# Optimization experiments

Measured on AMD Instinct MI355X. Metric: run time of the kernel, lower is better.

Reference implementation:

```python
import jax, jax.numpy as jnp
import numpy as np

BN_EPS = 1e-5
N_OUT, D_OUT = 64, 128


def setup_inputs() -> dict:
    key = jax.random.key(0)
    k1, k2, k3, k4 = jax.random.split(key, 4)
    B, N_in, D_in, K = 512, 64, 128, 4
    x = jax.random.normal(k1, (B, N_in, D_in), dtype=jnp.float32)
    # block-sparse weights: one (D_in x D_out) block per (output-row, active-input-row) pair
    W = jax.random.normal(k2, (N_OUT, K, D_in, D_OUT), dtype=jnp.float32) * (1.0 / np.sqrt(K * D_in))
    bias = jax.random.normal(k3, (N_OUT, D_OUT), dtype=jnp.float32) * 0.02
    gamma = jnp.ones((N_OUT * D_OUT,), dtype=jnp.float32)
    beta = jnp.zeros((N_OUT * D_OUT,), dtype=jnp.float32)
    idx = jax.random.randint(k4, (N_OUT, K), 0, N_in, dtype=jnp.int32)
    return {"x": x, "W": W, "bias": bias, "gamma": gamma, "beta": beta, "idx": idx}


def reference(x, W, bias, gamma, beta, idx):
    B = x.shape[0]
    # structured-sparse linear: gather active input rows, per-block matmul
    xg = x[:, idx, :]                                   # [B, N_out, K, D_in]
    y = jnp.einsum('bokd,okde->boe', xg, W) + bias      # [B, N_out, D_out]
    # BatchNorm1d (training-mode batch statistics) on flattened features
    yf = y.reshape(B, -1)                               # [B, N_out*D_out]
    mean = jnp.mean(yf, axis=0)
    var = jnp.mean(jnp.square(yf - mean), axis=0)       # biased variance, as in torch BN
    yn = (yf - mean) * jax.lax.rsqrt(var + BN_EPS) * gamma + beta
    # Swish: z * sigmoid(z)
    out = yn * jax.nn.sigmoid(yn)
    return out.reshape(B, N_OUT, D_OUT)
```

## Files before the change

kernel.cpp:

```cpp
#include <hip/hip_runtime.h>


typedef __attribute__((ext_vector_type(8))) __bf16 bf16x8;
typedef __attribute__((ext_vector_type(4))) __bf16 bf16x4;
typedef __attribute__((ext_vector_type(4))) float  f32x4;

#define B_SZ   512
#define N_IN   64
#define D_IN   128
#define N_O    64
#define D_O    128
#define FEAT   (N_O * D_O)
#define LDA    40

__global__ __launch_bounds__(1024, 4)
void fused_encoder_kernel(const float* __restrict__ x, const float* __restrict__ W,
                          const float* __restrict__ bias, const float* __restrict__ gamma,
                          const float* __restrict__ beta, const int* __restrict__ idxp,
                          float* __restrict__ out)
{
    __shared__ __bf16 Alds[512 * LDA];
    __shared__ __bf16 Blds[128 * LDA];
    __shared__ float  Sred[8 * 128];
    __shared__ float  Qred[8 * 128];
    __shared__ float  sscale[128];
    __shared__ float  sshift[128];

    const int o    = blockIdx.x;
    const int tid  = threadIdx.x;
    const int wave = tid >> 6;
    const int lane = tid & 63;
    const int wr   = wave >> 1;
    const int wc   = wave & 1;
    const int lam  = lane & 15;
    const int quad = lane >> 4;

    int rsel[4];
#pragma unroll
    for (int k = 0; k < 4; ++k) rsel[k] = idxp[o * 4 + k];

    const f32x4 zero4 = {0.f, 0.f, 0.f, 0.f};
    f32x4 acc[4][4];
#pragma unroll
    for (int mi = 0; mi < 4; ++mi)
#pragma unroll
        for (int ni = 0; ni < 4; ++ni) acc[mi][ni] = zero4;

    const int m_a = tid >> 1;
    const int ca  = (tid & 1) * 16;
    const int e_b = tid & 127;
    const int dgb = tid >> 7;

    for (int kk = 0; kk < 16; ++kk) {
        const int kidx = kk >> 2;
        const int d0   = (kk & 3) * 32;
        const int r    = rsel[kidx];

        const float* xa = x + ((m_a * N_IN + r) * D_IN + d0 + ca);
        f32x4 xv0 = *(const f32x4*)(xa + 0);
        f32x4 xv1 = *(const f32x4*)(xa + 4);
        f32x4 xv2 = *(const f32x4*)(xa + 8);
        f32x4 xv3 = *(const f32x4*)(xa + 12);
        bf16x8 p0, p1;
        p0[0] = (__bf16)xv0[0]; p0[1] = (__bf16)xv0[1];
        p0[2] = (__bf16)xv0[2]; p0[3] = (__bf16)xv0[3];
        p0[4] = (__bf16)xv1[0]; p0[5] = (__bf16)xv1[1];
        p0[6] = (__bf16)xv1[2]; p0[7] = (__bf16)xv1[3];
        p1[0] = (__bf16)xv2[0]; p1[1] = (__bf16)xv2[1];
        p1[2] = (__bf16)xv2[2]; p1[3] = (__bf16)xv2[3];
        p1[4] = (__bf16)xv3[0]; p1[5] = (__bf16)xv3[1];
        p1[6] = (__bf16)xv3[2]; p1[7] = (__bf16)xv3[3];

        const float* wp = W + (((o * 4 + kidx) * 128 + (d0 + dgb * 4)) * 128 + e_b);
        bf16x4 wb;
        wb[0] = (__bf16)wp[0];
        wb[1] = (__bf16)wp[128];
        wb[2] = (__bf16)wp[256];
        wb[3] = (__bf16)wp[384];

        __syncthreads();
        *(bf16x8*)&Alds[m_a * LDA + ca]     = p0;
        *(bf16x8*)&Alds[m_a * LDA + ca + 8] = p1;
        *(bf16x4*)&Blds[e_b * LDA + dgb * 4] = wb;
        __syncthreads();

        bf16x8 af[4], bfv[4];
#pragma unroll
        for (int mi = 0; mi < 4; ++mi)
            af[mi] = *(const bf16x8*)&Alds[(wr * 64 + mi * 16 + lam) * LDA + quad * 8];
#pragma unroll
        for (int ni = 0; ni < 4; ++ni)
            bfv[ni] = *(const bf16x8*)&Blds[(wc * 64 + ni * 16 + lam) * LDA + quad * 8];
#pragma unroll
        for (int mi = 0; mi < 4; ++mi)
#pragma unroll
            for (int ni = 0; ni < 4; ++ni)
                acc[mi][ni] = __builtin_amdgcn_mfma_f32_16x16x32_bf16(
                    af[mi], bfv[ni], acc[mi][ni], 0, 0, 0);
    }

    const int nbase = wc * 64;
    float bvals[4];
#pragma unroll
    for (int ni = 0; ni < 4; ++ni)
        bvals[ni] = bias[o * 128 + nbase + ni * 16 + lam];
#pragma unroll
    for (int mi = 0; mi < 4; ++mi)
#pragma unroll
        for (int ni = 0; ni < 4; ++ni)
#pragma unroll
            for (int rr = 0; rr < 4; ++rr) acc[mi][ni][rr] += bvals[ni];

#pragma unroll
    for (int ni = 0; ni < 4; ++ni) {
        float s = 0.f, q = 0.f;
#pragma unroll
        for (int mi = 0; mi < 4; ++mi)
#pragma unroll
            for (int rr = 0; rr < 4; ++rr) {
                const float v = acc[mi][ni][rr];
                s += v; q += v * v;
            }
        s += __shfl_xor(s, 16); s += __shfl_xor(s, 32);
        q += __shfl_xor(q, 16); q += __shfl_xor(q, 32);
        if (quad == 0) {
            const int e = nbase + ni * 16 + lam;
            Sred[wr * 128 + e] = s;
            Qred[wr * 128 + e] = q;
        }
    }
    __syncthreads();

    if (tid < 128) {
        float s = 0.f, q = 0.f;
#pragma unroll
        for (int sl = 0; sl < 8; ++sl) {
            s += Sred[sl * 128 + tid];
            q += Qred[sl * 128 + tid];
        }
        const float mean = s * (1.0f / 512.0f);
        const float var  = q * (1.0f / 512.0f) - mean * mean;
        const float rstd = rsqrtf(var + 1e-5f);
        const float sc   = rstd * gamma[o * 128 + tid];
        sscale[tid] = sc;
        sshift[tid] = beta[o * 128 + tid] - mean * sc;
    }
    __syncthreads();

#pragma unroll
    for (int mi = 0; mi < 4; ++mi) {
        const int rowb = wr * 64 + mi * 16 + quad * 4;
#pragma unroll
        for (int ni = 0; ni < 4; ++ni) {
            const int col = nbase + ni * 16 + lam;
            const float sc = sscale[col];
            const float sh = sshift[col];
#pragma unroll
            for (int rr = 0; rr < 4; ++rr) {
                const float xn = acc[mi][ni][rr] * sc + sh;
                const float sg = 1.0f / (1.0f + __expf(-xn));
                out[(rowb + rr) * FEAT + o * 128 + col] = xn * sg;
            }
        }
    }
}

extern "C" void kernel_launch(void* const* d_in, const int* in_sizes, int n_in,
                              void* d_out, int out_size, void* d_ws, size_t ws_size,
                              hipStream_t stream)
{
    const float* x     = (const float*)d_in[0];
    const float* W     = (const float*)d_in[1];
    const float* bias  = (const float*)d_in[2];
    const float* gamma = (const float*)d_in[3];
    const float* beta  = (const float*)d_in[4];
    const int*   idx   = (const int*)d_in[5];
    float* out = (float*)d_out;

    fused_encoder_kernel<<<dim3(64), dim3(1024), 0, stream>>>(
        x, W, bias, gamma, beta, idx, out);
}
```

Before: 121.9 us.

## Split batch across blocks with cooperative grid sync and double-buffered LDS pipeline

The grid grows from 64 blocks of 1024 threads to 256 blocks of 256 threads, each covering 128 batch rows for one output row. This spreads work over more CUs on the 256-CU part. BatchNorm partial sums now go to a global workspace and are combined after a cooperative grid-wide sync, with a block-to-output mapping chosen to keep XCD locality. The K loop is also double-buffered, prefetching global loads into registers two stages ahead. The cost is a grid barrier and global traffic for the statistics, plus each W block being loaded by four separate blocks.

```diff
diff --git a/kernel.cpp b/kernel.cpp
--- a/kernel.cpp
+++ b/kernel.cpp
@@ -1,32 +1,42 @@
 #include <hip/hip_runtime.h>
+#include <hip/hip_cooperative_groups.h>
+
+namespace cg = cooperative_groups;
 
 
 typedef __attribute__((ext_vector_type(8))) __bf16 bf16x8;
 typedef __attribute__((ext_vector_type(4))) __bf16 bf16x4;
 typedef __attribute__((ext_vector_type(4))) float  f32x4;
 
-#define B_SZ   512
 #define N_IN   64
 #define D_IN   128
-#define N_O    64
-#define D_O    128
-#define FEAT   (N_O * D_O)
+#define FEAT   8192
 #define LDA    40
 
-__global__ __launch_bounds__(1024, 4)
-void fused_encoder_kernel(const float* __restrict__ x, const float* __restrict__ W,
-                          const float* __restrict__ bias, const float* __restrict__ gamma,
-                          const float* __restrict__ beta, const int* __restrict__ idxp,
-                          float* __restrict__ out)
+struct Stage {
+    f32x4 a[4];
+    f32x4 w[4];
+};
+
+__global__ __launch_bounds__(256, 1)
+void fused_encoder_coop(const float* __restrict__ x, const float* __restrict__ W,
+                        const float* __restrict__ bias, const float* __restrict__ gamma,
+                        const float* __restrict__ beta, const int* __restrict__ idxp,
+                        float* __restrict__ out, float* __restrict__ psum,
+                        float* __restrict__ psq)
 {
-    __shared__ __bf16 Alds[512 * LDA];
-    __shared__ __bf16 Blds[128 * LDA];
-    __shared__ float  Sred[8 * 128];
-    __shared__ float  Qred[8 * 128];
+    __shared__ __bf16 Alds[2][128 * LDA];
+    __shared__ __bf16 Blds[2][128 * LDA];
     __shared__ float  sscale[128];
     __shared__ float  sshift[128];
 
-    const int o    = blockIdx.x;
+    const int bid = blockIdx.x;
+    const int xcd = bid & 7;
+    const int jj  = bid >> 3;
+    const int o   = (jj >> 2) * 8 + xcd;
+    const int bt  = jj & 3;
+    const int b0  = bt * 128;
+
     const int tid  = threadIdx.x;
     const int wave = tid >> 6;
     const int lane = tid & 63;
@@ -48,55 +58,85 @@
 
     const int m_a = tid >> 1;
     const int ca  = (tid & 1) * 16;
-    const int e_b = tid & 127;
-    const int dgb = tid >> 7;
-
-    for (int kk = 0; kk < 16; ++kk) {
-        const int kidx = kk >> 2;
-        const int d0   = (kk & 3) * 32;
-        const int r    = rsel[kidx];
-
-        const float* xa = x + ((m_a * N_IN + r) * D_IN + d0 + ca);
-        f32x4 xv0 = *(const f32x4*)(xa + 0);
-        f32x4 xv1 = *(const f32x4*)(xa + 4);
-        f32x4 xv2 = *(const f32x4*)(xa + 8);
-        f32x4 xv3 = *(const f32x4*)(xa + 12);
+    int te[4], tdg[4];
+#pragma unroll
+    for (int it = 0; it < 4; ++it) {
+        const int task = it * 256 + tid;
+        te[it]  = task & 127;
+        tdg[it] = task >> 7;
+    }
+
+    Stage s0, s1;
+
+    auto load_stage = [&](Stage& S, const int kkc) {
+        const int kidx = kkc >> 2;
+        const int d0   = (kkc & 3) * 32;
+        const float* xa = x + (((b0 + m_a) * N_IN + rsel[kidx]) * D_IN + d0 + ca);
+#pragma unroll
+        for (int v = 0; v < 4; ++v) S.a[v] = *(const f32x4*)(xa + v * 4);
+        const float* wb = W + (((o * 4 + kidx) * 128 + d0) * 128);
+#pragma unroll
+        for (int it = 0; it < 4; ++it) {
+            const float* wp = wb + tdg[it] * 4 * 128 + te[it];
+            f32x4 t;
+            t[0] = wp[0]; t[1] = wp[128]; t[2] = wp[256]; t[3] = wp[384];
+            S.w[it] = t;
+        }
+    };
+
+    auto store_stage = [&](const Stage& S, const int buf) {
         bf16x8 p0, p1;
-        p0[0] = (__bf16)xv0[0]; p0[1] = (__bf16)xv0[1];
-        p0[2] = (__bf16)xv0[2]; p0[3] = (__bf16)xv0[3];
-        p0[4] = (__bf16)xv1[0]; p0[5] = (__bf16)xv1[1];
-        p0[6] = (__bf16)xv1[2]; p0[7] = (__bf16)xv1[3];
-        p1[0] = (__bf16)xv2[0]; p1[1] = (__bf16)xv2[1];
-        p1[2] = (__bf16)xv2[2]; p1[3] = (__bf16)xv2[3];
-        p1[4] = (__bf16)xv3[0]; p1[5] = (__bf16)xv3[1];
-        p1[6] = (__bf16)xv3[2]; p1[7] = (__bf16)xv3[3];
-
-        const float* wp = W + (((o * 4 + kidx) * 128 + (d0 + dgb * 4)) * 128 + e_b);
-        bf16x4 wb;
-        wb[0] = (__bf16)wp[0];
-        wb[1] = (__bf16)wp[128];
-        wb[2] = (__bf16)wp[256];
-        wb[3] = (__bf16)wp[384];
-
-        __syncthreads();
-        *(bf16x8*)&Alds[m_a * LDA + ca]     = p0;
-        *(bf16x8*)&Alds[m_a * LDA + ca + 8] = p1;
-        *(bf16x4*)&Blds[e_b * LDA + dgb * 4] = wb;
-        __syncthreads();
-
+#pragma unroll
+        for (int j = 0; j < 4; ++j) {
+            p0[j]     = (__bf16)S.a[0][j];
+            p0[j + 4] = (__bf16)S.a[1][j];
+            p1[j]     = (__bf16)S.a[2][j];
+            p1[j + 4] = (__bf16)S.a[3][j];
+        }
+        *(bf16x8*)&Alds[buf][m_a * LDA + ca]     = p0;
+        *(bf16x8*)&Alds[buf][m_a * LDA + ca + 8] = p1;
+#pragma unroll
+        for (int it = 0; it < 4; ++it) {
+            bf16x4 q;
+#pragma unroll
+            for (int j = 0; j < 4; ++j) q[j] = (__bf16)S.w[it][j];
+            *(bf16x4*)&Blds[buf][te[it] * LDA + tdg[it] * 4] = q;
+        }
+    };
+
+    auto compute = [&](const int buf) {
         bf16x8 af[4], bfv[4];
 #pragma unroll
         for (int mi = 0; mi < 4; ++mi)
-            af[mi] = *(const bf16x8*)&Alds[(wr * 64 + mi * 16 + lam) * LDA + quad * 8];
+            af[mi] = *(const bf16x8*)&Alds[buf][(wr * 64 + mi * 16 + lam) * LDA + quad * 8];
 #pragma unroll
         for (int ni = 0; ni < 4; ++ni)
-            bfv[ni] = *(const bf16x8*)&Blds[(wc * 64 + ni * 16 + lam) * LDA + quad * 8];
+            bfv[ni] = *(const bf16x8*)&Blds[buf][(wc * 64 + ni * 16 + lam) * LDA + quad * 8];
 #pragma unroll
         for (int mi = 0; mi < 4; ++mi)
 #pragma unroll
             for (int ni = 0; ni < 4; ++ni)
                 acc[mi][ni] = __builtin_amdgcn_mfma_f32_16x16x32_bf16(
                     af[mi], bfv[ni], acc[mi][ni], 0, 0, 0);
+    };
+
+    load_stage(s0, 0);
+    load_stage(s1, 1);
+    store_stage(s0, 0);
+    __syncthreads();
+
+#pragma unroll
+    for (int kk = 0; kk < 16; ++kk) {
+        if (kk + 2 < 16) {
+            if (kk & 1) load_stage(s1, kk + 2);
+            else        load_stage(s0, kk + 2);
+        }
+        compute(kk & 1);
+        if (kk + 1 < 16) {
+            if (kk & 1) store_stage(s0, (kk + 1) & 1);
+            else        store_stage(s1, (kk + 1) & 1);
+            __syncthreads();
+        }
     }
 
     const int nbase = wc * 64;
@@ -124,19 +164,22 @@
         s += __shfl_xor(s, 16); s += __shfl_xor(s, 32);
         q += __shfl_xor(q, 16); q += __shfl_xor(q, 32);
         if (quad == 0) {
-            const int e = nbase + ni * 16 + lam;
-            Sred[wr * 128 + e] = s;
-            Qred[wr * 128 + e] = q;
-        }
-    }
-    __syncthreads();
+            const int slot = bt * 2 + wr;
+            const int e    = nbase + ni * 16 + lam;
+            psum[(o * 8 + slot) * 128 + e] = s;
+            psq [(o * 8 + slot) * 128 + e] = q;
+        }
+    }
+
+    __threadfence();
+    cg::this_grid().sync();
 
     if (tid < 128) {
         float s = 0.f, q = 0.f;
 #pragma unroll
         for (int sl = 0; sl < 8; ++sl) {
-            s += Sred[sl * 128 + tid];
-            q += Qred[sl * 128 + tid];
+            s += psum[(o * 8 + sl) * 128 + tid];
+            q += psq [(o * 8 + sl) * 128 + tid];
         }
         const float mean = s * (1.0f / 512.0f);
         const float var  = q * (1.0f / 512.0f) - mean * mean;
@@ -149,7 +192,7 @@
 
 #pragma unroll
     for (int mi = 0; mi < 4; ++mi) {
-        const int rowb = wr * 64 + mi * 16 + quad * 4;
+        const int rowb = b0 + wr * 64 + mi * 16 + quad * 4;
 #pragma unroll
         for (int ni = 0; ni < 4; ++ni) {
             const int col = nbase + ni * 16 + lam;
@@ -175,8 +218,11 @@
     const float* gamma = (const float*)d_in[3];
     const float* beta  = (const float*)d_in[4];
     const int*   idx   = (const int*)d_in[5];
-    float* out = (float*)d_out;
-
-    fused_encoder_kernel<<<dim3(64), dim3(1024), 0, stream>>>(
-        x, W, bias, gamma, beta, idx, out);
+    float* out  = (float*)d_out;
+    float* psum = (float*)d_ws;
+    float* psq  = psum + 64 * 8 * 128;
+
+    void* args[] = {&x, &W, &bias, &gamma, &beta, &idx, &out, &psum, &psq};
+    hipLaunchCooperativeKernel((const void*)fused_encoder_coop,
+                               dim3(256), dim3(256), args, 0, stream);
 }
```

Result: slower. 152.7 us (+25.3%).

## Split output columns across four blocks and double-buffer LDS with register prefetch

Applied to the files above, without the earlier changes.

Splits each output-row block's 128 columns into four 32-column slices, launching 256 workgroups instead of 64 so more of the GPU's compute units have work. Each wave now computes a 32x32 tile. The K loop is double-buffered: global loads for the stage two steps ahead are held in registers while the current LDS buffer is consumed, with one barrier per step instead of two. The cost is that each x row slice is now read by four blocks instead of one. Block IDs are remapped so the four slices of a row group are spread apart, and W is read with scalar loads.

```diff
diff --git a/kernel.cpp b/kernel.cpp
--- a/kernel.cpp
+++ b/kernel.cpp
@@ -2,36 +2,39 @@
 
 
 typedef __attribute__((ext_vector_type(8))) __bf16 bf16x8;
-typedef __attribute__((ext_vector_type(4))) __bf16 bf16x4;
 typedef __attribute__((ext_vector_type(4))) float  f32x4;
 
-#define B_SZ   512
-#define N_IN   64
-#define D_IN   128
-#define N_O    64
-#define D_O    128
-#define FEAT   (N_O * D_O)
-#define LDA    40
+#define FEAT 8192
+#define LDA  40
+
+#define PIPE_BARRIER() do { \
+    __builtin_amdgcn_sched_barrier(0); \
+    asm volatile("s_waitcnt lgkmcnt(0)" ::: "memory"); \
+    __builtin_amdgcn_s_barrier(); \
+    __builtin_amdgcn_sched_barrier(0); \
+} while (0)
 
 __global__ __launch_bounds__(1024, 4)
-void fused_encoder_kernel(const float* __restrict__ x, const float* __restrict__ W,
-                          const float* __restrict__ bias, const float* __restrict__ gamma,
-                          const float* __restrict__ beta, const int* __restrict__ idxp,
-                          float* __restrict__ out)
+void fused_encoder(const float* __restrict__ x, const float* __restrict__ W,
+                   const float* __restrict__ bias, const float* __restrict__ gamma,
+                   const float* __restrict__ beta, const int* __restrict__ idxp,
+                   float* __restrict__ out)
 {
-    __shared__ __bf16 Alds[512 * LDA];
-    __shared__ __bf16 Blds[128 * LDA];
-    __shared__ float  Sred[8 * 128];
-    __shared__ float  Qred[8 * 128];
-    __shared__ float  sscale[128];
-    __shared__ float  sshift[128];
+    __shared__ alignas(16) __bf16 Alds[2][512 * LDA];
+    __shared__ alignas(16) __bf16 Blds[2][32 * LDA];
+    __shared__ float Sred[16][32];
+    __shared__ float Qred[16][32];
+    __shared__ float sscale[32];
+    __shared__ float sshift[32];
 
-    const int o    = blockIdx.x;
+    const int bid = blockIdx.x;
+    const int o   = ((bid >> 5) << 3) | (bid & 7);
+    const int es  = (bid >> 3) & 3;
+    const int e0  = es * 32;
+
     const int tid  = threadIdx.x;
     const int wave = tid >> 6;
     const int lane = tid & 63;
-    const int wr   = wave >> 1;
-    const int wc   = wave & 1;
     const int lam  = lane & 15;
     const int quad = lane >> 4;
 
@@ -40,82 +43,95 @@
     for (int k = 0; k < 4; ++k) rsel[k] = idxp[o * 4 + k];
 
     const f32x4 zero4 = {0.f, 0.f, 0.f, 0.f};
-    f32x4 acc[4][4];
+    f32x4 acc[2][2];
 #pragma unroll
-    for (int mi = 0; mi < 4; ++mi)
+    for (int mi = 0; mi < 2; ++mi)
 #pragma unroll
-        for (int ni = 0; ni < 4; ++ni) acc[mi][ni] = zero4;
+        for (int ni = 0; ni < 2; ++ni) acc[mi][ni] = zero4;
 
     const int m_a = tid >> 1;
     const int ca  = (tid & 1) * 16;
-    const int e_b = tid & 127;
-    const int dgb = tid >> 7;
+    const int e_b = tid & 31;
+    const int d_b = tid >> 5;
 
+    f32x4 sA0[4], sA1[4];
+    float sB0, sB1;
+
+    auto load_stage = [&](f32x4 (&SA)[4], float& SB, const int kkc) {
+        const int kidx  = kkc >> 2;
+        const int dbase = (kkc & 3) * 32;
+        const float* xa = x + ((m_a * 64 + rsel[kidx]) * 128 + dbase + ca);
+#pragma unroll
+        for (int v = 0; v < 4; ++v) SA[v] = *(const f32x4*)(xa + v * 4);
+        SB = W[(((o * 4 + kidx) * 128) + dbase + d_b) * 128 + e0 + e_b];
+    };
+
+    auto store_stage = [&](const f32x4 (&SA)[4], const float SB, const int buf) {
+        bf16x8 p0, p1;
+#pragma unroll
+        for (int j = 0; j < 4; ++j) {
+            p0[j]     = (__bf16)SA[0][j];
+            p0[j + 4] = (__bf16)SA[1][j];
+            p1[j]     = (__bf16)SA[2][j];
+            p1[j + 4] = (__bf16)SA[3][j];
+        }
+        *(bf16x8*)&Alds[buf][m_a * LDA + ca]     = p0;
+        *(bf16x8*)&Alds[buf][m_a * LDA + ca + 8] = p1;
+        Blds[buf][e_b * LDA + d_b] = (__bf16)SB;
+    };
+
+    auto compute = [&](const int buf) {
+        bf16x8 af[2], bfr[2];
+#pragma unroll
+        for (int mi = 0; mi < 2; ++mi)
+            af[mi] = *(const bf16x8*)&Alds[buf][(wave * 32 + mi * 16 + lam) * LDA + quad * 8];
+#pragma unroll
+        for (int ni = 0; ni < 2; ++ni)
+            bfr[ni] = *(const bf16x8*)&Blds[buf][(ni * 16 + lam) * LDA + quad * 8];
+#pragma unroll
+        for (int mi = 0; mi < 2; ++mi)
+#pragma unroll
+            for (int ni = 0; ni < 2; ++ni)
+                acc[mi][ni] = __builtin_amdgcn_mfma_f32_16x16x32_bf16(
+                    af[mi], bfr[ni], acc[mi][ni], 0, 0, 0);
+    };
+
+    load_stage(sA0, sB0, 0);
+    load_stage(sA1, sB1, 1);
+    store_stage(sA0, sB0, 0);
+    PIPE_BARRIER();
+
+#pragma unroll
     for (int kk = 0; kk < 16; ++kk) {
-        const int kidx = kk >> 2;
-        const int d0   = (kk & 3) * 32;
-        const int r    = rsel[kidx];
-
-        const float* xa = x + ((m_a * N_IN + r) * D_IN + d0 + ca);
-        f32x4 xv0 = *(const f32x4*)(xa + 0);
-        f32x4 xv1 = *(const f32x4*)(xa + 4);
-        f32x4 xv2 = *(const f32x4*)(xa + 8);
-        f32x4 xv3 = *(const f32x4*)(xa + 12);
-        bf16x8 p0, p1;
-        p0[0] = (__bf16)xv0[0]; p0[1] = (__bf16)xv0[1];
-        p0[2] = (__bf16)xv0[2]; p0[3] = (__bf16)xv0[3];
-        p0[4] = (__bf16)xv1[0]; p0[5] = (__bf16)xv1[1];
-        p0[6] = (__bf16)xv1[2]; p0[7] = (__bf16)xv1[3];
-        p1[0] = (__bf16)xv2[0]; p1[1] = (__bf16)xv2[1];
-        p1[2] = (__bf16)xv2[2]; p1[3] = (__bf16)xv2[3];
-        p1[4] = (__bf16)xv3[0]; p1[5] = (__bf16)xv3[1];
-        p1[6] = (__bf16)xv3[2]; p1[7] = (__bf16)xv3[3];
-
-        const float* wp = W + (((o * 4 + kidx) * 128 + (d0 + dgb * 4)) * 128 + e_b);
-        bf16x4 wb;
-        wb[0] = (__bf16)wp[0];
-        wb[1] = (__bf16)wp[128];
-        wb[2] = (__bf16)wp[256];
-        wb[3] = (__bf16)wp[384];
-
-        __syncthreads();
-        *(bf16x8*)&Alds[m_a * LDA + ca]     = p0;
-        *(bf16x8*)&Alds[m_a * LDA + ca + 8] = p1;
-        *(bf16x4*)&Blds[e_b * LDA + dgb * 4] = wb;
-        __syncthreads();
-
-        bf16x8 af[4], bfv[4];
-#pragma unroll
-        for (int mi = 0; mi < 4; ++mi)
-            af[mi] = *(const bf16x8*)&Alds[(wr * 64 + mi * 16 + lam) * LDA + quad * 8];
-#pragma unroll
-        for (int ni = 0; ni < 4; ++ni)
-            bfv[ni] = *(const bf16x8*)&Blds[(wc * 64 + ni * 16 + lam) * LDA + quad * 8];
-#pragma unroll
-        for (int mi = 0; mi < 4; ++mi)
-#pragma unroll
-            for (int ni = 0; ni < 4; ++ni)
-                acc[mi][ni] = __builtin_amdgcn_mfma_f32_16x16x32_bf16(
-                    af[mi], bfv[ni], acc[mi][ni], 0, 0, 0);
+        if (kk + 2 < 16) {
+            if ((kk & 1) == 0) load_stage(sA0, sB0, kk + 2);
+            else               load_stage(sA1, sB1, kk + 2);
+        }
+        __builtin_amdgcn_sched_barrier(0);
+        compute(kk & 1);
+        if (kk + 1 < 16) {
+            if ((kk & 1) == 0) store_stage(sA1, sB1, 1);
+            else               store_stage(sA0, sB0, 0);
+            PIPE_BARRIER();
+        }
     }
 
-    const int nbase = wc * 64;
-    float bvals[4];
+    float bvals[2];
 #pragma unroll
-    for (int ni = 0; ni < 4; ++ni)
-        bvals[ni] = bias[o * 128 + nbase + ni * 16 + lam];
+    for (int ni = 0; ni < 2; ++ni)
+        bvals[ni] = bias[o * 128 + e0 + ni * 16 + lam];
 #pragma unroll
-    for (int mi = 0; mi < 4; ++mi)
+    for (int mi = 0; mi < 2; ++mi)
 #pragma unroll
-        for (int ni = 0; ni < 4; ++ni)
+        for (int ni = 0; ni < 2; ++ni)
 #pragma unroll
             for (int rr = 0; rr < 4; ++rr) acc[mi][ni][rr] += bvals[ni];
 
 #pragma unroll
-    for (int ni = 0; ni < 4; ++ni) {
+    for (int ni = 0; ni < 2; ++ni) {
         float s = 0.f, q = 0.f;
 #pragma unroll
-        for (int mi = 0; mi < 4; ++mi)
+        for (int mi = 0; mi < 2; ++mi)
 #pragma unroll
             for (int rr = 0; rr < 4; ++rr) {
                 const float v = acc[mi][ni][rr];
@@ -124,42 +140,41 @@
         s += __shfl_xor(s, 16); s += __shfl_xor(s, 32);
         q += __shfl_xor(q, 16); q += __shfl_xor(q, 32);
         if (quad == 0) {
-            const int e = nbase + ni * 16 + lam;
-            Sred[wr * 128 + e] = s;
-            Qred[wr * 128 + e] = q;
+            Sred[wave][ni * 16 + lam] = s;
+            Qred[wave][ni * 16 + lam] = q;
         }
     }
     __syncthreads();
 
-    if (tid < 128) {
+    if (tid < 32) {
         float s = 0.f, q = 0.f;
 #pragma unroll
-        for (int sl = 0; sl < 8; ++sl) {
-            s += Sred[sl * 128 + tid];
-            q += Qred[sl * 128 + tid];
+        for (int w = 0; w < 16; ++w) {
+            s += Sred[w][tid];
+            q += Qred[w][tid];
         }
         const float mean = s * (1.0f / 512.0f);
         const float var  = q * (1.0f / 512.0f) - mean * mean;
         const float rstd = rsqrtf(var + 1e-5f);
-        const float sc   = rstd * gamma[o * 128 + tid];
+        const float sc   = rstd * gamma[o * 128 + e0 + tid];
         sscale[tid] = sc;
-        sshift[tid] = beta[o * 128 + tid] - mean * sc;
+        sshift[tid] = beta[o * 128 + e0 + tid] - mean * sc;
     }
     __syncthreads();
 
 #pragma unroll
-    for (int mi = 0; mi < 4; ++mi) {
-        const int rowb = wr * 64 + mi * 16 + quad * 4;
+    for (int mi = 0; mi < 2; ++mi) {
+        const int rowb = wave * 32 + mi * 16 + quad * 4;
 #pragma unroll
-        for (int ni = 0; ni < 4; ++ni) {
-            const int col = nbase + ni * 16 + lam;
+        for (int ni = 0; ni < 2; ++ni) {
+            const int col = ni * 16 + lam;
             const float sc = sscale[col];
             const float sh = sshift[col];
 #pragma unroll
             for (int rr = 0; rr < 4; ++rr) {
                 const float xn = acc[mi][ni][rr] * sc + sh;
                 const float sg = 1.0f / (1.0f + __expf(-xn));
-                out[(rowb + rr) * FEAT + o * 128 + col] = xn * sg;
+                out[(rowb + rr) * FEAT + o * 128 + e0 + col] = xn * sg;
             }
         }
     }
@@ -177,6 +192,6 @@
     const int*   idx   = (const int*)d_in[5];
     float* out = (float*)d_out;
 
-    fused_encoder_kernel<<<dim3(64), dim3(1024), 0, stream>>>(
+    fused_encoder<<<dim3(256), dim3(1024), 0, stream>>>(
         x, W, bias, gamma, beta, idx, out);
 }
```

New measurement: 104.0 us. 14.7% less time.
